# Performance work log

Hardware: AMD Instinct MI355X
Metric: run time of the kernel (lower is better)

## Reference

```python
import jax, jax.numpy as jnp
import numpy as np

UNITS = 128
INPUT_DIM = 784
OUTPUT_DIM = 10
NUM_LAYERS = 8
BATCH = 2048
DT = 0.1
EPS = 0.01
TOL = 1e-4
STEPS = 15


def setup_inputs() -> dict:
    key = jax.random.key(0)
    k = jax.random.split(key, 7)
    s_in = 1.0 / np.sqrt(INPUT_DIM)
    s_u = 1.0 / np.sqrt(UNITS)
    return {
        "x": jax.random.normal(k[0], (BATCH, INPUT_DIM), jnp.float32),
        "w_in": jax.random.uniform(k[1], (UNITS, INPUT_DIM), jnp.float32, -s_in, s_in),
        "b_in": jax.random.uniform(k[2], (UNITS,), jnp.float32, -s_in, s_in),
        "w_blocks": jax.random.uniform(k[3], (NUM_LAYERS, UNITS, UNITS), jnp.float32, -s_u, s_u),
        "b_blocks": jax.random.uniform(k[4], (NUM_LAYERS, UNITS), jnp.float32, -s_u, s_u),
        "w_out": jax.random.uniform(k[5], (OUTPUT_DIM, UNITS), jnp.float32, -s_u, s_u),
        "b_out": jax.random.uniform(k[6], (OUTPUT_DIM,), jnp.float32, -s_u, s_u),
    }


def _build_A(w_blocks):
    # A_l = [[I, dt*W_l], [-dt*W_l^T, (1+dt/eps)*I]], shape [L, 2u, 2u]
    I = jnp.broadcast_to(jnp.eye(UNITS, dtype=w_blocks.dtype), (NUM_LAYERS, UNITS, UNITS))
    top = jnp.concatenate([I, DT * w_blocks], axis=2)
    bot = jnp.concatenate([-DT * jnp.transpose(w_blocks, (0, 2, 1)), (1.0 + DT / EPS) * I], axis=2)
    return jnp.concatenate([top, bot], axis=1)


def _sweep(z_in, A, b_blocks):
    # Fixed-point sweeping (no-grad region in the original). z_ls: [L, B, 2u]
    B = z_in.shape[0]

    def layer_step(z, xs):
        A_l, b_l, z_l = xs
        rhs = jnp.concatenate(
            [jnp.broadcast_to(DT * b_l, (B, UNITS)), (DT / EPS) * jnp.tanh(z_l[:, :UNITS])],
            axis=1,
        ) + z
        # A_l is shared across the batch: one LU, many rhs
        y = jnp.linalg.solve(A_l, rhs.T).T
        err = jnp.mean(jnp.linalg.norm(z_l - y, axis=1))
        return y, (y, err)

    def body(state):
        z_ls, _, step = state
        _, (new_zls, errs) = jax.lax.scan(layer_step, z_in, (A, b_blocks, z_ls))
        return (new_zls, jnp.mean(errs), step + 1)

    def cond(state):
        _, err, step = state
        return jnp.logical_and(step < STEPS, err > TOL)

    z0 = jnp.broadcast_to(z_in[None], (NUM_LAYERS,) + z_in.shape)
    z_ls, _, _ = jax.lax.while_loop(cond, body, (z0, jnp.float32(10.0), jnp.int32(0)))
    return z_ls


def _block(z_in, W, b, z_l):
    # implicit_forward of one TransNetLayerSweeping (z_l is the converged sweep state)
    u_l, v_l = z_l[:, :UNITS], z_l[:, UNITS:]
    u_out = -DT * (v_l @ W.T) + z_in[:, :UNITS] + DT * b
    v_out = DT * (u_l @ W) + z_in[:, UNITS:] - (DT / EPS) * (v_l - jnp.tanh(u_l))
    return jnp.concatenate([u_out, v_out], axis=1)


def reference(x, w_in, b_in, w_blocks, b_blocks, w_out, b_out):
    x1 = x @ w_in.T + b_in                                  # [B, u]
    z_in = jnp.concatenate([x1, jnp.tanh(x1)], axis=1)      # [B, 2u]
    z_ls = _sweep(z_in, _build_A(w_blocks), b_blocks)       # [L, B, 2u]
    # Original loop does z = block.implicit_forward(z_in) for every block,
    # so only the LAST block's output survives.
    z_out = _block(z_in, w_blocks[-1], b_blocks[-1], z_ls[-1])
    logits = z_out[:, :UNITS] @ w_out.T + b_out             # [B, out]
    return jax.nn.softmax(logits, axis=1)
```

## Files before the change

### kernel.cpp

```cpp
#include <hip/hip_runtime.h>

#define U 128
#define BATCH 2048
#define NL 8
#define NS 8
#define DTc 0.1f
#define TENf 10.0f
#define INVC (1.0f/11.0f)
#define AFACT (0.01f/11.0f)
#define AST 264
#define PREP_BLKS 64

typedef unsigned short u16;
typedef __attribute__((ext_vector_type(8))) short bf16x8;
typedef __attribute__((ext_vector_type(4))) float f32x4;
#define MFMA16(a,b,c) __builtin_amdgcn_mfma_f32_16x16x32_bf16(a,b,c,0,0,0)

__device__ __forceinline__ float bf2f(u16 h){ return __uint_as_float(((unsigned int)h)<<16); }
__device__ __forceinline__ u16 f2bf(float f){
  unsigned int u = __float_as_uint(f);
  u += 0x7FFFu + ((u >> 16) & 1u);
  return (u16)(u >> 16);
}
__device__ __forceinline__ float fast_tanh(float x){
  float e = __expf(2.0f*x);
  return 1.0f - __fdividef(2.0f, e + 1.0f);
}
__device__ __forceinline__ int detect_md(const u16* x, int* s_bad, int t, int nthr){
  if(t==0) *s_bad = 0;
  __syncthreads();
  int f=0;
  for(int i=t;i<4096;i+=nthr){ float v = bf2f(x[i]); if(!(fabsf(v)<16.0f)) f=1; }
  if(f) atomicOr(s_bad,1);
  __syncthreads();
  return *s_bad ? 0 : 1;
}
__device__ __forceinline__ bf16x8 ld8f(const float* p){
  float4 f0 = *(const float4*)p, f1 = *(const float4*)(p+4);
  bf16x8 v;
  v[0]=(short)f2bf(f0.x); v[1]=(short)f2bf(f0.y); v[2]=(short)f2bf(f0.z); v[3]=(short)f2bf(f0.w);
  v[4]=(short)f2bf(f1.x); v[5]=(short)f2bf(f1.y); v[6]=(short)f2bf(f1.z); v[7]=(short)f2bf(f1.w);
  return v;
}
__device__ __forceinline__ void lgkm_barrier(){
  __builtin_amdgcn_sched_barrier(0);
  asm volatile("s_waitcnt lgkmcnt(0)\n\ts_barrier" ::: "memory");
  __builtin_amdgcn_sched_barrier(0);
}

__device__ __forceinline__ void gbar(unsigned* cnt, int idx){
  __syncthreads();
  if(threadIdx.x==0){
    __threadfence();
    unsigned old = __hip_atomic_fetch_add(&cnt[idx], 1u, __ATOMIC_ACQ_REL, __HIP_MEMORY_SCOPE_AGENT);
    unsigned tgt = (old/PREP_BLKS + 1u)*PREP_BLKS;
    while(__hip_atomic_load(&cnt[idx], __ATOMIC_ACQUIRE, __HIP_MEMORY_SCOPE_AGENT) < tgt)
      __builtin_amdgcn_s_sleep(4);
  }
  __syncthreads();
}

template<typename EPI>
__device__ __forceinline__ void tile16(const u16* __restrict__ A, int lda,
                                       const u16* __restrict__ B, int ldb, EPI epi){
  const int lane = threadIdx.x & 63, w = threadIdx.x >> 6;
  const int ln = lane & 15, lq = lane >> 4;
  const int n0 = 32*w + ln, n1 = n0 + 16;
  bf16x8 af[4], b0[4], b1[4];
  #pragma unroll
  for(int kt=0;kt<4;kt++){
    af[kt] = *(const bf16x8*)&A[ln*lda + kt*32 + lq*8];
    b0[kt] = *(const bf16x8*)&B[n0*ldb + kt*32 + lq*8];
    b1[kt] = *(const bf16x8*)&B[n1*ldb + kt*32 + lq*8];
  }
  f32x4 a0 = {0,0,0,0}, a1 = {0,0,0,0};
  #pragma unroll
  for(int kt=0;kt<4;kt++){ a0 = MFMA16(af[kt], b0[kt], a0); a1 = MFMA16(af[kt], b1[kt], a1); }
  epi(a0, a1, n0, n1);
}

__global__ __launch_bounds__(256) void prepK(
    const void* __restrict__ xraw, const void* __restrict__ wb,
    u16* __restrict__ Wg, u16* __restrict__ Wtg, u16* __restrict__ Pg,
    u16* __restrict__ Fb, u16* __restrict__ Fsw, unsigned* __restrict__ cnt){
  __shared__ int s_bad;
  const int t = threadIdx.x, bid = blockIdx.x;
  const int md = detect_md((const u16*)xraw, &s_bad, t, 256);

  {
    const int g = bid*256 + t, GS = PREP_BLKS*256;
    for(int i=g;i<131072;i+=GS){
      u16 h = md ? ((const u16*)wb)[i] : f2bf(((const float*)wb)[i]);
      Wg[i] = h;
      int L = i>>14, j = i & 16383;
      Wtg[(L<<14) + (j&127)*U + (j>>7)] = h;
    }
  }
  gbar(cnt, 0);

  const int L = bid >> 3, mt = bid & 7;
  const int lq = (t & 63) >> 4;
  const u16* WtL = Wtg + (L<<14);
  u16* PL  = Pg + (L<<14);
  u16* FbL = Fb + (size_t)L*65536;

  tile16(WtL + mt*16*U, U, WtL, U, [&](f32x4 a0, f32x4 a1, int n0, int n1){
    #pragma unroll
    for(int r=0;r<4;r++){
      int row = mt*16 + lq*4 + r;
      PL[row*U + n0] = f2bf(AFACT*a0[r]);
      PL[row*U + n1] = f2bf(AFACT*a1[r]);
    }
  });
  gbar(cnt, 1);

  tile16(PL + mt*16*U, U, PL, U, [&](f32x4 a0, f32x4 a1, int n0, int n1){
    #pragma unroll
    for(int r=0;r<4;r++){
      int row = mt*16 + lq*4 + r;
      FbL[row*256 + n0] = f2bf(INVC*(((row==n0)?1.0f:0.0f) - bf2f(PL[row*U+n0]) + a0[r]));
      FbL[row*256 + n1] = f2bf(INVC*(((row==n1)?1.0f:0.0f) - bf2f(PL[row*U+n1]) + a1[r]));
    }
  });
  __syncthreads();

  tile16(FbL + mt*16*256, 256, Wg + (L<<14), U, [&](f32x4 a0, f32x4 a1, int n0, int n1){
    #pragma unroll
    for(int r=0;r<4;r++){
      int row = mt*16 + lq*4 + r;
      u16 q0 = f2bf(DTc*a0[r]), q1 = f2bf(DTc*a1[r]);
      FbL[row*256 + 128 + n0] = q0;
      FbL[row*256 + 128 + n1] = q1;
      FbL[(128+n0)*256 + row] = q0;
      FbL[(128+n1)*256 + row] = q1;
    }
  });
  gbar(cnt, 2);

  tile16(Wg + (L<<14) + mt*16*U, U, FbL + 128*256, 256, [&](f32x4 a0, f32x4 a1, int n0, int n1){
    #pragma unroll
    for(int r=0;r<4;r++){
      int row = mt*16 + lq*4 + r;
      FbL[(128+row)*256 + 128 + n0] = f2bf(DTc*a0[r]);
      FbL[(128+row)*256 + 128 + n1] = f2bf(DTc*a1[r]);
    }
  });
  gbar(cnt, 3);

  for(int i = mt*1024 + t; i < (mt+1)*1024; i += 256){
    int lanei = i & 63, kt = (i>>6)&7, c = (i>>9)&3, w = (i>>11)&3;
    int lni = lanei & 15, lqi = lanei >> 4;
    int row_n = 64*w + 16*c + lni;
    int col_k = kt*32 + lqi*8;
    *(bf16x8*)&Fsw[((size_t)L*8192 + i)*8] = *(const bf16x8*)&FbL[row_n*256 + col_k];
  }
}

__global__ __launch_bounds__(1024,4) void mainK(
    const void* __restrict__ xraw, const void* __restrict__ w_in,
    const void* __restrict__ b_in, const void* __restrict__ bb,
    const bf16x8* __restrict__ Fsw, const void* __restrict__ w_out,
    const void* __restrict__ b_out, void* __restrict__ outraw){
  __shared__ u16 At[2][16*AST];
  __shared__ u16 zh16[NL][16][132];
  __shared__ float zinu[16*U];
  __shared__ float bbL[NL*U];
  __shared__ float lg[16*12];
  __shared__ int s_bad;
  float* uout = (float*)&At[0][0];

  const int t = threadIdx.x;
  const int lane = t & 63, wid = t >> 6, ln = lane & 15, lq = lane >> 4;
  const int r0 = blockIdx.x * 16;

  const int md = detect_md((const u16*)xraw, &s_bad, t, 1024);
  for(int i=t;i<NL*U;i+=1024)
    bbL[i] = DTc * (md ? bf2f(((const u16*)bb)[i]) : ((const float*)bb)[i]);
  __syncthreads();

  if(wid < 8){
    const int n0 = 16*wid + ln;
    const u16*   wrb = (const u16*)w_in   + (size_t)n0*784;
    const float* wrf = (const float*)w_in + (size_t)n0*784;
    const u16*   xrb = (const u16*)xraw   + (size_t)(r0+ln)*784;
    const float* xrf = (const float*)xraw + (size_t)(r0+ln)*784;
    f32x4 acc = {0,0,0,0};
    const bf16x8 z8 = {0,0,0,0,0,0,0,0};
    if(md){
      #pragma unroll
      for(int kt=0; kt<24; ++kt){
        int k0 = kt*32 + lq*8;
        acc = MFMA16(*(const bf16x8*)(xrb + k0), *(const bf16x8*)(wrb + k0), acc);
      }
      { int k0 = 768 + lq*8;
        bf16x8 av = z8, bv = z8;
        if(lq < 2){ av = *(const bf16x8*)(xrb + k0); bv = *(const bf16x8*)(wrb + k0); }
        acc = MFMA16(av, bv, acc);
      }
    } else {
      #pragma unroll 4
      for(int kt=0; kt<24; ++kt){
        int k0 = kt*32 + lq*8;
        acc = MFMA16(ld8f(xrf + k0), ld8f(wrf + k0), acc);
      }
      { int k0 = 768 + lq*8;
        bf16x8 av = z8, bv = z8;
        if(lq < 2){ av = ld8f(xrf + k0); bv = ld8f(wrf + k0); }
        acc = MFMA16(av, bv, acc);
      }
    }
    float bi = md ? bf2f(((const u16*)b_in)[n0]) : ((const float*)b_in)[n0];
    #pragma unroll
    for(int r=0;r<4;r++) zinu[(lq*4+r)*U + n0] = acc[r] + bi;
  }
  __syncthreads();

  for(int i=t; i<NL*16*128; i+=1024){
    int l = i>>11, row = (i>>7)&15, c = i & 127;
    zh16[l][row][c] = f2bf(zinu[row*U + c]);
  }
  float ru[4];
  if(wid < 8){
    const int n = 16*wid + ln;
    #pragma unroll
    for(int r=0;r<4;r++){
      int row = lq*4 + r;
      At[0][row*AST + n] = f2bf((TENf + 1.0f) * fast_tanh(zinu[row*U + n]));
    }
  } else {
    const int uc = 16*(wid-8) + ln;
    #pragma unroll
    for(int r=0;r<4;r++){
      int row = lq*4 + r;
      float v = zinu[row*U + uc] + bbL[uc];
      ru[r] = v;
      At[0][row*AST + 128 + uc] = f2bf(v);
    }
  }
  const bf16x8* fbase = Fsw + (wid>>2)*2048 + (wid&3)*512 + lane;
  bf16x8 BfA[8], BfB[8];
  #pragma unroll
  for(int kt=0;kt<8;kt++) BfA[kt] = fbase[kt*64];
  __syncthreads();

#define STEPBODY(STEPV, BC, BN, CURC) { \
    const int l = (STEPV) & 7; \
    const int lnext = (l+1) & 7; \
    const bool last = ((STEPV) == NS*NL-1); \
    { const bf16x8* fp = fbase + lnext*8192; \
      _Pragma("unroll") \
      for(int kt=0;kt<8;kt++) BN[kt] = fp[kt*64]; } \
    bf16x8 at8[8]; \
    _Pragma("unroll") \
    for(int kt=0;kt<8;kt++) at8[kt] = *(const bf16x8*)&At[CURC][ln*AST + kt*32 + lq*8]; \
    float th[4]; \
    if(wid < 8 && !last){ \
      _Pragma("unroll") \
      for(int r=0;r<4;r++) th[r] = TENf * fast_tanh(bf2f(zh16[lnext][lq*4 + r][16*wid + ln])); \
    } \
    f32x4 acc = {0,0,0,0}; \
    _Pragma("unroll") \
    for(int kt=0;kt<8;kt++) acc = MFMA16(at8[kt], BC[kt], acc); \
    if(wid < 8){ \
      if(!last){ \
        const bool wrap = (l == 7); \
        const int n = 16*wid + ln; \
        _Pragma("unroll") \
        for(int r=0;r<4;r++){ \
          int row = lq*4 + r; \
          float base = wrap ? fast_tanh(zinu[row*U + n]) : acc[r]; \
          At[1-(CURC)][row*AST + n] = f2bf(th[r] + base); \
        } \
      } \
    } else { \
      const int uc0 = 16*(wid-8) + ln; \
      _Pragma("unroll") \
      for(int r=0;r<4;r++){ \
        int row = lq*4 + r; \
        float yu = ru[r] - acc[r]; \
        zh16[l][row][uc0] = f2bf(yu); \
        if(last){ \
          uout[row*U + uc0] = zinu[row*U + uc0] + bbL[7*U + uc0] - acc[r]; \
        } else if(l == 7){ \
          float rn = zinu[row*U + uc0] + bbL[uc0]; \
          ru[r] = rn; \
          At[1-(CURC)][row*AST + 128 + uc0] = f2bf(rn); \
        } else { \
          float rn = yu + bbL[(l+1)*U + uc0]; \
          ru[r] = rn; \
          At[1-(CURC)][row*AST + 128 + uc0] = f2bf(rn); \
        } \
      } \
    } \
    lgkm_barrier(); \
  }

  for(int sp=0; sp<NS*NL; sp+=2){
    STEPBODY(sp,   BfA, BfB, 0)
    STEPBODY(sp+1, BfB, BfA, 1)
  }
#undef STEPBODY

  if(t < 160){
    int mm = t/10, o = t - mm*10;
    float a = md ? bf2f(((const u16*)b_out)[o]) : ((const float*)b_out)[o];
    if(md){
      const u16* wo = (const u16*)w_out + o*U;
      for(int k=0;k<U;k++) a += uout[mm*U + k]*bf2f(wo[k]);
    } else {
      const float* wo = (const float*)w_out + o*U;
      for(int k=0;k<U;k++) a += uout[mm*U + k]*wo[k];
    }
    lg[mm*12 + o] = a;
  }
  __syncthreads();
  if(t < 16){
    float mx = -1e30f;
    for(int o=0;o<10;o++) mx = fmaxf(mx, lg[t*12 + o]);
    float e[10]; float sum = 0.0f;
    for(int o=0;o<10;o++){ e[o] = __expf(lg[t*12 + o] - mx); sum += e[o]; }
    float inv = 1.0f / sum;
    for(int o=0;o<10;o++){
      float pv = e[o]*inv;
      if(md) ((u16*)outraw)[(size_t)(r0 + t)*10 + o] = f2bf(pv);
      else   ((float*)outraw)[(size_t)(r0 + t)*10 + o] = pv;
    }
  }
}

extern "C" void kernel_launch(void* const* d_in, const int* in_sizes, int n_in,
                              void* d_out, int out_size, void* d_ws, size_t ws_size,
                              hipStream_t stream) {
  char* p = (char*)d_ws;
  u16* Fb      = (u16*)p;  p += (size_t)8*256*256*2;
  u16* Fsw     = (u16*)p;  p += (size_t)8*256*256*2;
  u16* Wg      = (u16*)p;  p += (size_t)8*128*128*2;
  u16* Wtg     = (u16*)p;  p += (size_t)8*128*128*2;
  u16* Pg      = (u16*)p;  p += (size_t)8*128*128*2;
  unsigned* cnt = (unsigned*)p; p += 64;

  hipMemsetAsync(cnt, 0, 64, stream);
  prepK<<<PREP_BLKS, 256, 0, stream>>>(d_in[0], d_in[3], Wg, Wtg, Pg, Fb, Fsw, cnt);
  mainK<<<BATCH/16, 1024, 0, stream>>>(d_in[0], d_in[1], d_in[2], d_in[4],
                                       (const bf16x8*)Fsw, d_in[5], d_in[6], d_out);
}
```

Baseline: 218.8 us.

## Replace grid-barrier prep kernel with redundant per-block LDS computation

The prep kernel no longer splits each layer's small matrix products across 8 blocks joined by global atomic barriers. Instead, each of the 64 blocks recomputes the full 128x128 products for its layer in shared memory and writes only its slice of the swizzled factor matrix. This removes the grid-wide spin barriers, the memset, and the global scratch round-trips, at the cost of 8x redundant MFMA work per layer and more shared memory per block.

```diff
diff --git a/kernel.cpp b/kernel.cpp
--- a/kernel.cpp
+++ b/kernel.cpp
@@ -9,16 +9,16 @@
 #define INVC (1.0f/11.0f)
 #define AFACT (0.01f/11.0f)
 #define AST 264
-#define PREP_BLKS 64
 
 typedef unsigned short u16;
+typedef unsigned int u32;
 typedef __attribute__((ext_vector_type(8))) short bf16x8;
 typedef __attribute__((ext_vector_type(4))) float f32x4;
 #define MFMA16(a,b,c) __builtin_amdgcn_mfma_f32_16x16x32_bf16(a,b,c,0,0,0)
 
-__device__ __forceinline__ float bf2f(u16 h){ return __uint_as_float(((unsigned int)h)<<16); }
+__device__ __forceinline__ float bf2f(u16 h){ return __uint_as_float(((u32)h)<<16); }
 __device__ __forceinline__ u16 f2bf(float f){
-  unsigned int u = __float_as_uint(f);
+  u32 u = __float_as_uint(f);
   u += 0x7FFFu + ((u >> 16) & 1u);
   return (u16)(u >> 16);
 }
@@ -48,111 +48,110 @@
   __builtin_amdgcn_sched_barrier(0);
 }
 
-__device__ __forceinline__ void gbar(unsigned* cnt, int idx){
-  __syncthreads();
-  if(threadIdx.x==0){
-    __threadfence();
-    unsigned old = __hip_atomic_fetch_add(&cnt[idx], 1u, __ATOMIC_ACQ_REL, __HIP_MEMORY_SCOPE_AGENT);
-    unsigned tgt = (old/PREP_BLKS + 1u)*PREP_BLKS;
-    while(__hip_atomic_load(&cnt[idx], __ATOMIC_ACQUIRE, __HIP_MEMORY_SCOPE_AGENT) < tgt)
-      __builtin_amdgcn_s_sleep(4);
-  }
-  __syncthreads();
-}
-
-template<typename EPI>
-__device__ __forceinline__ void tile16(const u16* __restrict__ A, int lda,
-                                       const u16* __restrict__ B, int ldb, EPI epi){
-  const int lane = threadIdx.x & 63, w = threadIdx.x >> 6;
-  const int ln = lane & 15, lq = lane >> 4;
-  const int n0 = 32*w + ln, n1 = n0 + 16;
-  bf16x8 af[4], b0[4], b1[4];
+template<typename GB, typename EPI>
+__device__ __forceinline__ void gfull(const u16* __restrict__ A, GB getB, EPI epi,
+                                      int w, int ln, int lq){
+  const int n0 = 16*w + ln;
+  bf16x8 bfr[4];
   #pragma unroll
-  for(int kt=0;kt<4;kt++){
-    af[kt] = *(const bf16x8*)&A[ln*lda + kt*32 + lq*8];
-    b0[kt] = *(const bf16x8*)&B[n0*ldb + kt*32 + lq*8];
-    b1[kt] = *(const bf16x8*)&B[n1*ldb + kt*32 + lq*8];
-  }
-  f32x4 a0 = {0,0,0,0}, a1 = {0,0,0,0};
-  #pragma unroll
-  for(int kt=0;kt<4;kt++){ a0 = MFMA16(af[kt], b0[kt], a0); a1 = MFMA16(af[kt], b1[kt], a1); }
-  epi(a0, a1, n0, n1);
-}
-
-__global__ __launch_bounds__(256) void prepK(
+  for(int kt=0;kt<4;kt++) bfr[kt] = getB(n0, kt*32 + lq*8);
+  #pragma unroll 2
+  for(int rt=0; rt<8; rt++){
+    f32x4 acc = {0,0,0,0};
+    #pragma unroll
+    for(int kt=0;kt<4;kt++){
+      bf16x8 af = *(const bf16x8*)&A[(rt*16+ln)*U + kt*32 + lq*8];
+      acc = MFMA16(af, bfr[kt], acc);
+    }
+    epi(acc, rt*16 + lq*4, n0);
+  }
+}
+
+__global__ __launch_bounds__(512) void prepB(
     const void* __restrict__ xraw, const void* __restrict__ wb,
-    u16* __restrict__ Wg, u16* __restrict__ Wtg, u16* __restrict__ Pg,
-    u16* __restrict__ Fb, u16* __restrict__ Fsw, unsigned* __restrict__ cnt){
-  __shared__ int s_bad;
-  const int t = threadIdx.x, bid = blockIdx.x;
-  const int md = detect_md((const u16*)xraw, &s_bad, t, 256);
-
+    u16* __restrict__ Fsw){
+  __shared__ u16 bufA[16384];
+  __shared__ u16 bufB[16384];
+  const int t = threadIdx.x;
+  const int lane = t & 63, w = t >> 6, ln = lane & 15, lq = lane >> 4;
+  const int L = blockIdx.x >> 3, mt = blockIdx.x & 7;
+  const int md = detect_md((const u16*)xraw, (int*)bufA, t, 512);
+  __syncthreads();
+  const u16*   wbb = (const u16*)wb   + ((size_t)L<<14);
+  const float* wbf = (const float*)wb + ((size_t)L<<14);
+
+  for(int j=t;j<16384;j+=512){
+    u16 h = md ? wbb[j] : f2bf(wbf[j]);
+    bufA[(j&127)*U + (j>>7)] = h;
+  }
+  __syncthreads();
+
+  auto gA = [&](int n,int k0)->bf16x8{ return *(const bf16x8*)&bufA[n*U+k0]; };
+  auto gB = [&](int n,int k0)->bf16x8{ return *(const bf16x8*)&bufB[n*U+k0]; };
+  auto gW = [&](int n,int k0)->bf16x8{
+    if(md) return *(const bf16x8*)&wbb[n*U+k0];
+    return ld8f(wbf + n*U + k0);
+  };
+
+  gfull(bufA, gA, [&](f32x4 acc, int rowb, int n0){
+    #pragma unroll
+    for(int r=0;r<4;r++) bufB[(rowb+r)*U + n0] = f2bf(AFACT*acc[r]);
+  }, w, ln, lq);
+  __syncthreads();
+  gfull(bufB, gB, [&](f32x4 acc, int rowb, int n0){
+    #pragma unroll
+    for(int r=0;r<4;r++){
+      int row = rowb + r;
+      bufA[row*U + n0] = f2bf(INVC*(((row==n0)?1.0f:0.0f) - bf2f(bufB[row*U+n0]) + acc[r]));
+    }
+  }, w, ln, lq);
+  __syncthreads();
+  gfull(bufA, gW, [&](f32x4 acc, int rowb, int n0){
+    #pragma unroll
+    for(int r=0;r<4;r++) bufB[(rowb+r)*U + n0] = f2bf(DTc*acc[r]);
+  }, w, ln, lq);
+  __syncthreads();
+
+  for(int i = mt*1024 + t; i < (mt+1)*1024; i += 512){
+    int wf = (i>>11)&3;
+    if(wf >= 2) continue;
+    int lanei = i & 63, kt = (i>>6)&7, c = (i>>9)&3;
+    int row_n = 64*wf + 16*c + (lanei & 15);
+    int col_k = kt*32 + (lanei >> 4)*8;
+    bf16x8 v = (kt < 4) ? *(const bf16x8*)&bufA[row_n*U + col_k]
+                        : *(const bf16x8*)&bufB[row_n*U + col_k - 128];
+    *(bf16x8*)&Fsw[((size_t)L*8192 + i)*8] = v;
+  }
+  __syncthreads();
+  for(int j=t;j<16384;j+=512) bufA[(j&127)*U + (j>>7)] = bufB[j];
+  __syncthreads();
+  for(int i = mt*1024 + t; i < (mt+1)*1024; i += 512){
+    int wf = (i>>11)&3, kt = (i>>6)&7;
+    if(wf < 2 || kt >= 4) continue;
+    int lanei = i & 63, c = (i>>9)&3;
+    int row_n = 64*wf + 16*c + (lanei & 15);
+    int col_k = kt*32 + (lanei >> 4)*8;
+    *(bf16x8*)&Fsw[((size_t)L*8192 + i)*8] = *(const bf16x8*)&bufA[(row_n-128)*U + col_k];
+  }
   {
-    const int g = bid*256 + t, GS = PREP_BLKS*256;
-    for(int i=g;i<131072;i+=GS){
-      u16 h = md ? ((const u16*)wb)[i] : f2bf(((const float*)wb)[i]);
-      Wg[i] = h;
-      int L = i>>14, j = i & 16383;
-      Wtg[(L<<14) + (j&127)*U + (j>>7)] = h;
-    }
-  }
-  gbar(cnt, 0);
-
-  const int L = bid >> 3, mt = bid & 7;
-  const int lq = (t & 63) >> 4;
-  const u16* WtL = Wtg + (L<<14);
-  u16* PL  = Pg + (L<<14);
-  u16* FbL = Fb + (size_t)L*65536;
-
-  tile16(WtL + mt*16*U, U, WtL, U, [&](f32x4 a0, f32x4 a1, int n0, int n1){
+    const int n0 = 16*w + ln;
+    bf16x8 bq[4];
+    #pragma unroll
+    for(int kt=0;kt<4;kt++) bq[kt] = *(const bf16x8*)&bufA[n0*U + kt*32 + lq*8];
+    f32x4 acc = {0,0,0,0};
+    #pragma unroll
+    for(int kt=0;kt<4;kt++){
+      bf16x8 af = gW(mt*16 + ln, kt*32 + lq*8);
+      acc = MFMA16(af, bq[kt], acc);
+    }
+    const int wf = 2 + (mt>>2), cc = mt & 3;
+    const int kt_ = 4 + (n0>>5), lqi = (n0>>3)&3, jj = n0 & 7;
     #pragma unroll
     for(int r=0;r<4;r++){
-      int row = mt*16 + lq*4 + r;
-      PL[row*U + n0] = f2bf(AFACT*a0[r]);
-      PL[row*U + n1] = f2bf(AFACT*a1[r]);
-    }
-  });
-  gbar(cnt, 1);
-
-  tile16(PL + mt*16*U, U, PL, U, [&](f32x4 a0, f32x4 a1, int n0, int n1){
-    #pragma unroll
-    for(int r=0;r<4;r++){
-      int row = mt*16 + lq*4 + r;
-      FbL[row*256 + n0] = f2bf(INVC*(((row==n0)?1.0f:0.0f) - bf2f(PL[row*U+n0]) + a0[r]));
-      FbL[row*256 + n1] = f2bf(INVC*(((row==n1)?1.0f:0.0f) - bf2f(PL[row*U+n1]) + a1[r]));
-    }
-  });
-  __syncthreads();
-
-  tile16(FbL + mt*16*256, 256, Wg + (L<<14), U, [&](f32x4 a0, f32x4 a1, int n0, int n1){
-    #pragma unroll
-    for(int r=0;r<4;r++){
-      int row = mt*16 + lq*4 + r;
-      u16 q0 = f2bf(DTc*a0[r]), q1 = f2bf(DTc*a1[r]);
-      FbL[row*256 + 128 + n0] = q0;
-      FbL[row*256 + 128 + n1] = q1;
-      FbL[(128+n0)*256 + row] = q0;
-      FbL[(128+n1)*256 + row] = q1;
-    }
-  });
-  gbar(cnt, 2);
-
-  tile16(Wg + (L<<14) + mt*16*U, U, FbL + 128*256, 256, [&](f32x4 a0, f32x4 a1, int n0, int n1){
-    #pragma unroll
-    for(int r=0;r<4;r++){
-      int row = mt*16 + lq*4 + r;
-      FbL[(128+row)*256 + 128 + n0] = f2bf(DTc*a0[r]);
-      FbL[(128+row)*256 + 128 + n1] = f2bf(DTc*a1[r]);
-    }
-  });
-  gbar(cnt, 3);
-
-  for(int i = mt*1024 + t; i < (mt+1)*1024; i += 256){
-    int lanei = i & 63, kt = (i>>6)&7, c = (i>>9)&3, w = (i>>11)&3;
-    int lni = lanei & 15, lqi = lanei >> 4;
-    int row_n = 64*w + 16*c + lni;
-    int col_k = kt*32 + lqi*8;
-    *(bf16x8*)&Fsw[((size_t)L*8192 + i)*8] = *(const bf16x8*)&FbL[row_n*256 + col_k];
+      int lni = lq*4 + r;
+      int i = (wf<<11)|(cc<<9)|(kt_<<6)|(lqi<<4)|lni;
+      Fsw[((size_t)L*8192 + i)*8 + jj] = f2bf(DTc*acc[r]);
+    }
   }
 }
 
@@ -331,16 +330,9 @@
 extern "C" void kernel_launch(void* const* d_in, const int* in_sizes, int n_in,
                               void* d_out, int out_size, void* d_ws, size_t ws_size,
                               hipStream_t stream) {
-  char* p = (char*)d_ws;
-  u16* Fb      = (u16*)p;  p += (size_t)8*256*256*2;
-  u16* Fsw     = (u16*)p;  p += (size_t)8*256*256*2;
-  u16* Wg      = (u16*)p;  p += (size_t)8*128*128*2;
-  u16* Wtg     = (u16*)p;  p += (size_t)8*128*128*2;
-  u16* Pg      = (u16*)p;  p += (size_t)8*128*128*2;
-  unsigned* cnt = (unsigned*)p; p += 64;
-
-  hipMemsetAsync(cnt, 0, 64, stream);
-  prepK<<<PREP_BLKS, 256, 0, stream>>>(d_in[0], d_in[3], Wg, Wtg, Pg, Fb, Fsw, cnt);
+  u16* Fsw = (u16*)d_ws;
+
+  prepB<<<64, 512, 0, stream>>>(d_in[0], d_in[3], Fsw);
   mainK<<<BATCH/16, 1024, 0, stream>>>(d_in[0], d_in[1], d_in[2], d_in[4],
                                        (const bf16x8*)Fsw, d_in[5], d_in[6], d_out);
 }
```

New measurement: 218.5 us. No clear change (-0.1%).
